# Kernel tuning notes

Measured on AMD Instinct MI355X. Metric: run time of the kernel, lower is better.

## Reference

```python
import jax, jax.numpy as jnp
import numpy as np

B, S, HID = 2, 4096, 1024
H, D = 16, 64

def rotate_half(x):
    x1, x2 = jnp.split(x, 2, axis=-1)
    return jnp.concatenate([-x2, x1], axis=-1)

def setup_inputs() -> dict:
    key = jax.random.key(0)
    ks = jax.random.split(key, 8)
    hidden_states = jax.random.normal(ks[0], (B, S, HID), dtype=jnp.float32)
    pos = jnp.arange(S, dtype=jnp.float32)[:, None]
    inv_freq = 1.0 / (10000.0 ** (jnp.arange(0, D, 2, dtype=jnp.float32) / D))
    freqs = pos * inv_freq[None, :]
    emb = jnp.concatenate([freqs, freqs], axis=-1)  # [S, D]
    cos = jnp.cos(emb)
    sin = jnp.sin(emb)
    W_rkv = jax.random.normal(ks[1], (3 * H * D, HID), dtype=jnp.float32) * 0.02
    W_o = jax.random.normal(ks[2], (HID, H * D), dtype=jnp.float32) * 0.02
    # match torch init: uniform(-8,-5), uniform(-1,1), uniform(0.2,0.8)
    time_decay = jax.random.uniform(ks[3], (H, D), minval=-8.0, maxval=-5.0, dtype=jnp.float32)
    time_first = jax.random.uniform(ks[4], (H, D), minval=-1.0, maxval=1.0, dtype=jnp.float32)
    time_mix = jax.random.uniform(ks[5], (1, 1, HID), minval=0.2, maxval=0.8, dtype=jnp.float32)
    return {"hidden_states": hidden_states, "cos": cos, "sin": sin,
            "W_rkv": W_rkv, "W_o": W_o, "time_decay": time_decay,
            "time_first": time_first, "time_mix": time_mix}

def reference(hidden_states, cos, sin, W_rkv, W_o, time_decay, time_first, time_mix):
    b, s, hid = hidden_states.shape
    # token-shift time mixing
    xx = jnp.concatenate([jnp.zeros_like(hidden_states[:, :1]), hidden_states[:, :-1]], axis=1)
    mixed = hidden_states * time_mix + xx * (1.0 - time_mix)
    rkv = jnp.einsum('bsh,oh->bso', mixed, W_rkv).reshape(b, s, 3, H, D)
    r = jax.nn.sigmoid(rkv[:, :, 0])  # [B,S,H,D]
    k = rkv[:, :, 1]
    v = rkv[:, :, 2]
    # rotary on r, k
    c = cos[None, :, None, :]
    sn = sin[None, :, None, :]
    r = r * c + rotate_half(r) * sn
    k = k * c + rotate_half(k) * sn
    # fast rwkv linear attention (parallel approximation)
    w = -jnp.exp(time_decay)
    kv = k * v  # [B,S,H,D]
    pos = jnp.arange(s, dtype=hidden_states.dtype)
    pos_diff = pos[:, None] - pos[None, :]  # [S,S]
    mask = pos_diff > 0  # i > j masked (per original code)
    avg_decay = jnp.mean(w)
    pd = jnp.where(mask, 0.0, pos_diff)
    dw = jnp.where(mask, 0.0, jnp.exp(avg_decay * -jnp.abs(pd)))
    dw = dw / (dw.sum(axis=1, keepdims=True) + 1e-8)
    weighted_kv = jnp.einsum('ij,bjhd->bihd', dw, kv)
    out = r * (time_first[None, None] * kv + weighted_kv)  # [B,S,H,D]
    out = out.reshape(b, s, H * D)
    return jnp.einsum('bso,ho->bsh', out, W_o)
```

## Files before the change

kernel.cpp:

```cpp
#include <hip/hip_runtime.h>
#include <math.h>

#define S_LEN 4096
#define HIDN  1024
#define NH    16
#define HD    64
#define BATCH 2
#define M_TOTAL (BATCH * S_LEN)
#define N_RKV   (3 * HIDN)
#define CS 128
#define NC (S_LEN / CS)

typedef __attribute__((ext_vector_type(8))) _Float16 f16x8;
typedef __attribute__((ext_vector_type(4))) float f32x4;
typedef __attribute__((ext_vector_type(4))) unsigned short u16x4;

__device__ __forceinline__ unsigned short f2h(float x) {
    _Float16 h = (_Float16)x;
    return *(unsigned short*)&h;
}
__device__ __forceinline__ float h2f(unsigned short b) {
    _Float16 h = *(_Float16*)&b;
    return (float)h;
}

__device__ __forceinline__ void load_lds16(const void* g, void* l) {
    __builtin_amdgcn_global_load_lds((const __attribute__((address_space(1))) void*)g,
                                     (__attribute__((address_space(3))) void*)l, 16, 0, 0);
}

__global__ void k_avg_decay(const float* __restrict__ td, float* __restrict__ a_out) {
    int t = threadIdx.x;
    double acc = 0.0;
    for (int i = t; i < NH * HD; i += 64) acc += exp((double)td[i]);
    for (int off = 32; off > 0; off >>= 1) acc += __shfl_down(acc, off, 64);
    if (t == 0) a_out[0] = (float)(acc / (double)(NH * HD));
}

__global__ __launch_bounds__(256)
void k_split_mix(const float* __restrict__ hs, const float* __restrict__ tm,
                 unsigned short* __restrict__ Ah) {
    int g = blockIdx.x * 256 + threadIdx.x;
    int kc = (g & 255) * 4;
    int m = g >> 8;
    float4 cur = *(const float4*)&hs[(size_t)m * HIDN + kc];
    float4 t4  = *(const float4*)&tm[kc];
    float4 prev = make_float4(0.f, 0.f, 0.f, 0.f);
    if (m & (S_LEN - 1)) prev = *(const float4*)&hs[(size_t)(m - 1) * HIDN + kc];
    u16x4 h;
    h.x = f2h(cur.x * t4.x + prev.x * (1.f - t4.x));
    h.y = f2h(cur.y * t4.y + prev.y * (1.f - t4.y));
    h.z = f2h(cur.z * t4.z + prev.z * (1.f - t4.z));
    h.w = f2h(cur.w * t4.w + prev.w * (1.f - t4.w));
    *(u16x4*)&Ah[(size_t)m * HIDN + kc] = h;
}

__global__ __launch_bounds__(256)
void k_split_w(const float* __restrict__ W, unsigned short* __restrict__ Wh) {
    int g = blockIdx.x * 256 + threadIdx.x;
    size_t o = (size_t)g * 4;
    float4 v = *(const float4*)&W[o];
    u16x4 h;
    h.x = f2h(v.x); h.y = f2h(v.y); h.z = f2h(v.z); h.w = f2h(v.w);
    *(u16x4*)&Wh[o] = h;
}

__device__ __forceinline__ f32x4 mfma16(f16x8 a, f16x8 b, f32x4 c) {
    return __builtin_amdgcn_mfma_f32_16x16x32_f16(a, b, c, 0, 0, 0);
}

template<int LDC, int NBX, bool HALF_OUT>
__global__ __launch_bounds__(256, 2)
void k_gemm_bt(const unsigned short* __restrict__ A,
               const unsigned short* __restrict__ Bm,
               void* __restrict__ Cv)
{
    __shared__ unsigned short smem[16384];
    const int tid  = threadIdx.x;
    const int lane = tid & 63;
    const int wave = tid >> 6;
    const int wm = wave >> 1, wn = wave & 1;

    const int cpx = gridDim.x >> 3;
    const int wg  = (blockIdx.x & 7) * cpx + (blockIdx.x >> 3);
    const int bx  = wg % NBX;
    const int by  = wg / NBX;
    const int m0 = by * 128;
    const int n0 = bx * 128;

    const unsigned short* segsrc[4];
    int segdst[4];
    {
        int rowoff = lane >> 2;
        int q = (lane & 3) ^ (rowoff & 3);
#pragma unroll
        for (int i = 0; i < 4; ++i) {
            int s = wave * 4 + i;
            const unsigned short* base = (s < 8) ? A : Bm;
            int row = (s < 8) ? (m0 + s * 16) : (n0 + (s - 8) * 16);
            segsrc[i] = base + (size_t)(row + rowoff) * 1024 + q * 8;
            segdst[i] = s * 512;
        }
    }

    const int lm = lane & 15;
    const int rq = lane >> 4;
    const int qx = rq ^ (lane & 3);
    int aoff[4], boff[4];
#pragma unroll
    for (int t = 0; t < 4; ++t) {
        aoff[t] = (wm * 64 + t * 16 + lm) * 32 + qx * 8;
        boff[t] = 4096 + (wn * 64 + t * 16 + lm) * 32 + qx * 8;
    }

    f32x4 acc[4][4] = {};

#pragma unroll
    for (int i = 0; i < 4; ++i) load_lds16(segsrc[i], smem + segdst[i]);

    int p = 0;
    for (int kt = 0; kt < 1024; kt += 32) {
        __syncthreads();
        if (kt + 32 < 1024) {
#pragma unroll
            for (int i = 0; i < 4; ++i)
                load_lds16(segsrc[i] + kt + 32, smem + ((p ^ 1) * 8192 + segdst[i]));
        }
        const unsigned short* sb = smem + p * 8192;
        f16x8 fa[4], fb[4];
#pragma unroll
        for (int t = 0; t < 4; ++t) {
            fa[t] = *(const f16x8*)(sb + aoff[t]);
            fb[t] = *(const f16x8*)(sb + boff[t]);
        }
#pragma unroll
        for (int mt = 0; mt < 4; ++mt)
#pragma unroll
            for (int nt = 0; nt < 4; ++nt)
                acc[mt][nt] = mfma16(fa[mt], fb[nt], acc[mt][nt]);
        p ^= 1;
    }

#pragma unroll
    for (int mt = 0; mt < 4; ++mt)
#pragma unroll
        for (int nt = 0; nt < 4; ++nt) {
            int col = n0 + wn * 64 + nt * 16 + lm;
#pragma unroll
            for (int r = 0; r < 4; ++r) {
                int row = m0 + wm * 64 + mt * 16 + rq * 4 + r;
                if constexpr (HALF_OUT)
                    ((unsigned short*)Cv)[(size_t)row * LDC + col] = f2h(acc[mt][nt][r]);
                else
                    ((float*)Cv)[(size_t)row * LDC + col] = acc[mt][nt][r];
            }
        }
}

__global__ __launch_bounds__(256)
void k_cb(const unsigned short* __restrict__ rkv,
          const float* __restrict__ cosp, const float* __restrict__ sinp,
          const float* __restrict__ a_ptr, float* __restrict__ Cb)
{
    __shared__ float Ls[4][64][4];
    int bid = blockIdx.x;
    int c  = bid & (NC - 1);
    int bh = bid >> 5;
    int b = bh >> 4, h = bh & 15;
    int lane = threadIdx.x & 63;
    int wave = threadIdx.x >> 6;
    int lm = lane & 15;
    int rs = lane >> 4;
    int d0 = lm * 4;
    float a = a_ptr[0];
    float sgn = (lm < 8) ? -1.f : 1.f;
    float ps0 = 0.f, ps1 = 0.f, ps2 = 0.f, ps3 = 0.f;
#pragma unroll
    for (int it = 0; it < 8; ++it) {
        int t = wave * 32 + it * 4 + rs;
        int s = c * CS + t;
        const unsigned short* rk = rkv + ((size_t)b * S_LEN + s) * N_RKV + h * 64 + d0;
        u16x4 k4 = *(const u16x4*)(rk + 1024);
        u16x4 v4 = *(const u16x4*)(rk + 2048);
        float4 cs4 = *(const float4*)&cosp[s * HD + d0];
        float4 sn4 = *(const float4*)&sinp[s * HD + d0];
        float e = expf(a * (float)t);
        float k0 = h2f(k4.x), k1 = h2f(k4.y), k2 = h2f(k4.z), k3 = h2f(k4.w);
        float kp0 = __shfl_xor(k0, 8, 64);
        float kp1 = __shfl_xor(k1, 8, 64);
        float kp2 = __shfl_xor(k2, 8, 64);
        float kp3 = __shfl_xor(k3, 8, 64);
        ps0 += e * (k0 * cs4.x + sgn * kp0 * sn4.x) * h2f(v4.x);
        ps1 += e * (k1 * cs4.y + sgn * kp1 * sn4.y) * h2f(v4.y);
        ps2 += e * (k2 * cs4.z + sgn * kp2 * sn4.z) * h2f(v4.z);
        ps3 += e * (k3 * cs4.w + sgn * kp3 * sn4.w) * h2f(v4.w);
    }
    Ls[wave][lane][0] = ps0; Ls[wave][lane][1] = ps1;
    Ls[wave][lane][2] = ps2; Ls[wave][lane][3] = ps3;
    __syncthreads();
    if (threadIdx.x < 64) {
        int d = threadIdx.x;
        int lmm = d >> 2, j = d & 3;
        float sum = 0.f;
#pragma unroll
        for (int wv = 0; wv < 4; ++wv)
#pragma unroll
            for (int r = 0; r < 4; ++r)
                sum += Ls[wv][r * 16 + lmm][j];
        Cb[((size_t)bh * NC + c) * 64 + d] = sum;
    }
}

__global__ __launch_bounds__(64)
void k_chunk_suffix(const float* __restrict__ Cb, const float* __restrict__ a_ptr,
                    float* __restrict__ Sb) {
    int bh = blockIdx.x;
    int d = threadIdx.x;
    float a = a_ptr[0];
    float eaCS = expf(a * (float)CS);
    float run = 0.f;
    Sb[(size_t)(bh * NC + NC - 1) * 64 + d] = 0.f;
    for (int c = NC - 2; c >= 0; --c) {
        run = Cb[(size_t)(bh * NC + c + 1) * 64 + d] + eaCS * run;
        Sb[(size_t)(bh * NC + c) * 64 + d] = run;
    }
}

__global__ __launch_bounds__(256)
void k_ztab(const float* __restrict__ a_ptr, float* __restrict__ Zt) {
    int i = blockIdx.x * 256 + threadIdx.x;
    if (i < S_LEN) {
        float a = a_ptr[0];
        float em1a = expm1f(a);
        Zt[i] = expm1f(a * (float)(S_LEN - i)) / em1a + 1e-8f;
    }
}

__global__ __launch_bounds__(256)
void k_wkv2(const unsigned short* __restrict__ rkv,
            const float* __restrict__ cosp, const float* __restrict__ sinp,
            const float* __restrict__ Sb, const float* __restrict__ a_ptr,
            const float* __restrict__ tf, const float* __restrict__ Zt,
            unsigned short* __restrict__ outH) {
    __shared__ unsigned short L[3 * 128 * 64];
    __shared__ float Tl[4][64];
    int bid = blockIdx.x;
    int c  = bid & (NC - 1);
    int bh = bid >> 5;
    int b = bh >> 4, h = bh & 15;
    int lane = threadIdx.x & 63;
    int wave = threadIdx.x >> 6;
    int s0 = c * CS;

#pragma unroll
    for (int i = 0; i < 12; ++i) {
        int seg = wave * 12 + i;
        int stream = seg >> 4;
        int rg = seg & 15;
        int row = rg * 8 + (lane >> 3);
        const unsigned short* src = rkv
            + ((size_t)b * S_LEN + s0 + row) * N_RKV + stream * 1024 + h * 64
            + (lane & 7) * 8;
        load_lds16(src, L + stream * 8192 + rg * 512);
    }
    __syncthreads();

    float a = a_ptr[0];
    float ea = expf(a);
    const unsigned short* Lr = L;
    const unsigned short* Lk = L + 8192;
    const unsigned short* Lv = L + 16384;
    float sgn = (lane < 32) ? -1.f : 1.f;
    int lx = lane ^ 32;

    float kvreg[32], rreg[32];
    float w = 1.f, T = 0.f;
#pragma unroll
    for (int t = 0; t < 32; ++t) {
        int row = wave * 32 + t;
        float r_ = h2f(Lr[row * 64 + lane]);
        float k_ = h2f(Lk[row * 64 + lane]);
        float kp = h2f(Lk[row * 64 + lx]);
        float v_ = h2f(Lv[row * 64 + lane]);
        float cs = cosp[(s0 + row) * HD + lane];
        float sn = sinp[(s0 + row) * HD + lane];
        float sig = 1.f / (1.f + expf(-r_));
        float sigp = __shfl_xor(sig, 32, 64);
        rreg[t]  = sig * cs + sgn * sigp * sn;
        kvreg[t] = (k_ * cs + sgn * kp * sn) * v_;
        T += w * kvreg[t];
        w *= ea;
    }
    Tl[wave][lane] = T;
    __syncthreads();

    float e32 = expf(a * 32.f);
    float S_run = Sb[(size_t)bid * 64 + lane] * expf(a * 32.f * (float)(3 - wave));
    float f = 1.f;
    for (int wp = wave + 1; wp < 4; ++wp) {
        S_run += f * Tl[wp][lane];
        f *= e32;
    }
    float tfv = tf[h * HD + lane];
#pragma unroll
    for (int t = 31; t >= 0; --t) {
        float kv = kvreg[t];
        S_run = kv + ea * S_run;
        int ig = s0 + wave * 32 + t;
        float Z = Zt[ig];
        float o = rreg[t] * (tfv * kv + S_run / Z);
        size_t m = (size_t)b * S_LEN + ig;
        outH[m * HIDN + h * HD + lane] = f2h(o);
    }
}

extern "C" void kernel_launch(void* const* d_in, const int* in_sizes, int n_in,
                              void* d_out, int out_size, void* d_ws, size_t ws_size,
                              hipStream_t stream) {
    const float* hs    = (const float*)d_in[0];
    const float* cosp  = (const float*)d_in[1];
    const float* sinp  = (const float*)d_in[2];
    const float* W_rkv = (const float*)d_in[3];
    const float* W_o   = (const float*)d_in[4];
    const float* td    = (const float*)d_in[5];
    const float* tf    = (const float*)d_in[6];
    const float* tm    = (const float*)d_in[7];
    float* out = (float*)d_out;

    char* w = (char*)d_ws;
    unsigned short* rkvH = (unsigned short*)w;
    unsigned short* Ah   = (unsigned short*)(w + 50331648);
    unsigned short* outH = (unsigned short*)(w + 50331648);
    unsigned short* Wrh  = (unsigned short*)(w + 67108864);
    unsigned short* Woh  = (unsigned short*)(w + 73400320);
    float*          Cb   = (float*)(w + 75497472);
    float*          Sb   = (float*)(w + 75759616);
    float*          a_ptr= (float*)(w + 76021760);
    float*          Zt   = Cb;

    k_avg_decay<<<1, 64, 0, stream>>>(td, a_ptr);

    k_split_mix<<<(M_TOTAL * HIDN / 4) / 256, 256, 0, stream>>>(hs, tm, Ah);
    k_split_w<<<(N_RKV * HIDN / 4) / 256, 256, 0, stream>>>(W_rkv, Wrh);
    k_split_w<<<(HIDN * HIDN / 4) / 256, 256, 0, stream>>>(W_o, Woh);

    k_gemm_bt<N_RKV, 24, true><<<1536, 256, 0, stream>>>(Ah, Wrh, rkvH);

    k_cb<<<BATCH * NH * NC, 256, 0, stream>>>(rkvH, cosp, sinp, a_ptr, Cb);
    k_chunk_suffix<<<BATCH * NH, 64, 0, stream>>>(Cb, a_ptr, Sb);
    k_ztab<<<S_LEN / 256, 256, 0, stream>>>(a_ptr, Zt);
    k_wkv2<<<BATCH * NH * NC, 256, 0, stream>>>(rkvH, cosp, sinp, Sb, a_ptr, tf, Zt, outH);

    k_gemm_bt<HIDN, 8, false><<<512, 256, 0, stream>>>(outH, Woh, out);
}
```

Baseline: 239.8 us.

## Replace RKV projection GEMM with 256x192-tile, 8-wave phased pipelined kernel

Adds a new 512-thread GEMM for the RKV projection that uses 256x192 output tiles with a 64-wide K step and double-buffered LDS. It interleaves async global-to-LDS staging with four MFMA phases per stage, using explicit waitcnt, sched barriers and setprio. The aim is to raise data reuse per tile and hide load latency better than the generic 128x128 kernel, at the cost of more LDS, register pressure and hand-tuned scheduling fragility. It also precomputes the reciprocal of the normalizer table so the WKV kernel multiplies instead of dividing.

```diff
diff --git a/kernel.cpp b/kernel.cpp
--- a/kernel.cpp
+++ b/kernel.cpp
@@ -69,6 +69,122 @@
     return __builtin_amdgcn_mfma_f32_16x16x32_f16(a, b, c, 0, 0, 0);
 }
 
+#define SBAR  do { __builtin_amdgcn_sched_barrier(0); __builtin_amdgcn_s_barrier(); \
+                   __builtin_amdgcn_sched_barrier(0); } while (0)
+#define LGKM0 do { asm volatile("s_waitcnt lgkmcnt(0)" ::: "memory"); \
+                   __builtin_amdgcn_sched_barrier(0); } while (0)
+#define VMC(n) asm volatile("s_waitcnt vmcnt(" #n ")" ::: "memory")
+
+__global__ __launch_bounds__(512, 2)
+void k_gemm1_8ph(const unsigned short* __restrict__ A,
+                 const unsigned short* __restrict__ Bm,
+                 unsigned short* __restrict__ C)
+{
+    __shared__ unsigned short smem[57344];
+    const int tid  = threadIdx.x;
+    const int lane = tid & 63;
+    const int wv   = tid >> 6;
+    const int wm = wv >> 2, wn = wv & 3;
+    const int lm = lane & 15, rq = lane >> 4;
+    const int swz = (lm & 7) << 4;
+
+    const int cpx = gridDim.x >> 3;
+    const int wg  = (blockIdx.x & 7) * cpx + (blockIdx.x >> 3);
+    const int bx  = wg & 15;
+    const int by  = wg >> 4;
+    const int m0 = by * 256, n0 = bx * 192;
+
+    const int srow = 8 * wv + (lane >> 3);
+    const int scol = ((lane & 7) ^ (lane >> 3)) * 8;
+    const unsigned short* sA = A  + (size_t)(m0 + srow) * 1024 + scol;
+    const unsigned short* sB = Bm + (size_t)(n0 + srow) * 1024 + scol;
+    unsigned short* dA = smem + wv * 512;
+    unsigned short* dB = smem + 16384 + wv * 512;
+
+#define STG_A(u, T, bf) load_lds16(sA + (u)*65536 + (T)*64, dA + (bf)*28672 + (u)*4096)
+#define STG_B(u, T, bf) load_lds16(sB + (u)*65536 + (T)*64, dB + (bf)*28672 + (u)*4096)
+
+    const int arow = (wm * 128 + lm) * 128 + rq * 16;
+    int boff[3][2];
+#pragma unroll
+    for (int nt = 0; nt < 3; ++nt)
+#pragma unroll
+        for (int kk = 0; kk < 2; ++kk)
+            boff[nt][kk] = (((wn * 48 + nt * 16 + lm) * 128 + rq * 16 + kk * 64) ^ swz);
+
+    f16x8 aF[2][2], bF[3][2];
+    f32x4 acc[8][3] = {};
+
+#define READ_A(q, bf) { const char* Ab = (const char*)smem + (bf)*57344; \
+    _Pragma("unroll") for (int m2 = 0; m2 < 2; ++m2) \
+    _Pragma("unroll") for (int kk = 0; kk < 2; ++kk) \
+        aF[m2][kk] = *(const f16x8*)(Ab + ((arow + (q)*4096 + m2*2048 + kk*64) ^ swz)); }
+
+#define READ_B(bf) { const char* Bb = (const char*)smem + (bf)*57344 + 32768; \
+    _Pragma("unroll") for (int nt = 0; nt < 3; ++nt) \
+    _Pragma("unroll") for (int kk = 0; kk < 2; ++kk) \
+        bF[nt][kk] = *(const f16x8*)(Bb + boff[nt][kk]); }
+
+#define MMQ(q) { __builtin_amdgcn_s_setprio(1); \
+    _Pragma("unroll") for (int kk = 0; kk < 2; ++kk) \
+    _Pragma("unroll") for (int m2 = 0; m2 < 2; ++m2) \
+    _Pragma("unroll") for (int nt = 0; nt < 3; ++nt) \
+        acc[(q)*2+m2][nt] = mfma16(aF[m2][kk], bF[nt][kk], acc[(q)*2+m2][nt]); \
+    __builtin_amdgcn_s_setprio(0); }
+
+    STG_A(0,0,0); STG_A(1,0,0); STG_A(2,0,0); STG_A(3,0,0);
+    STG_B(0,0,0); STG_B(1,0,0); STG_B(2,0,0);
+    STG_B(0,1,1); STG_B(1,1,1); STG_B(2,1,1);
+    STG_A(0,1,1); STG_A(2,1,1);
+    VMC(5);
+    SBAR;
+
+    for (int it = 0; it < 8; ++it) {
+        const int t = 2 * it;
+        const bool st = (it < 7);
+        READ_A(0, 0); READ_B(0);
+        STG_A(1, t + 1, 1); STG_A(3, t + 1, 1);
+        SBAR; LGKM0; MMQ(0); SBAR;
+        READ_A(1, 0);
+        if (st) { STG_B(0, t + 2, 0); STG_B(1, t + 2, 0); }
+        SBAR; LGKM0; MMQ(1); SBAR;
+        READ_A(2, 0);
+        if (st) { STG_B(2, t + 2, 0); STG_A(0, t + 2, 0); }
+        SBAR; LGKM0; MMQ(2); SBAR;
+        READ_A(3, 0);
+        if (st) { STG_A(2, t + 2, 0); }
+        SBAR; LGKM0; MMQ(3);
+        if (st) { VMC(5); } else { VMC(0); }
+        SBAR;
+        READ_A(0, 1); READ_B(1);
+        if (st) { STG_A(1, t + 2, 0); STG_A(3, t + 2, 0); }
+        SBAR; LGKM0; MMQ(0); SBAR;
+        READ_A(1, 1);
+        if (st) { STG_B(0, t + 3, 1); STG_B(1, t + 3, 1); }
+        SBAR; LGKM0; MMQ(1); SBAR;
+        READ_A(2, 1);
+        if (st) { STG_B(2, t + 3, 1); STG_A(0, t + 3, 1); }
+        SBAR; LGKM0; MMQ(2); SBAR;
+        READ_A(3, 1);
+        if (st) { STG_A(2, t + 3, 1); }
+        SBAR; LGKM0; MMQ(3);
+        if (st) { VMC(5); }
+        SBAR;
+    }
+
+#pragma unroll
+    for (int mt = 0; mt < 8; ++mt)
+#pragma unroll
+        for (int nt = 0; nt < 3; ++nt) {
+            int col = n0 + wn * 48 + nt * 16 + lm;
+#pragma unroll
+            for (int r = 0; r < 4; ++r) {
+                int row = m0 + wm * 128 + mt * 16 + rq * 4 + r;
+                C[(size_t)row * N_RKV + col] = f2h(acc[mt][nt][r]);
+            }
+        }
+}
+
 template<int LDC, int NBX, bool HALF_OUT>
 __global__ __launch_bounds__(256, 2)
 void k_gemm_bt(const unsigned short* __restrict__ A,
@@ -106,11 +222,11 @@
     const int lm = lane & 15;
     const int rq = lane >> 4;
     const int qx = rq ^ (lane & 3);
-    int aoff[4], boff[4];
+    int aoff[4], boff2[4];
 #pragma unroll
     for (int t = 0; t < 4; ++t) {
-        aoff[t] = (wm * 64 + t * 16 + lm) * 32 + qx * 8;
-        boff[t] = 4096 + (wn * 64 + t * 16 + lm) * 32 + qx * 8;
+        aoff[t]  = (wm * 64 + t * 16 + lm) * 32 + qx * 8;
+        boff2[t] = 4096 + (wn * 64 + t * 16 + lm) * 32 + qx * 8;
     }
 
     f32x4 acc[4][4] = {};
@@ -127,17 +243,17 @@
                 load_lds16(segsrc[i] + kt + 32, smem + ((p ^ 1) * 8192 + segdst[i]));
         }
         const unsigned short* sb = smem + p * 8192;
-        f16x8 fa[4], fb[4];
+        f16x8 fah[4], fb[4];
 #pragma unroll
         for (int t = 0; t < 4; ++t) {
-            fa[t] = *(const f16x8*)(sb + aoff[t]);
-            fb[t] = *(const f16x8*)(sb + boff[t]);
+            fah[t] = *(const f16x8*)(sb + aoff[t]);
+            fb[t]  = *(const f16x8*)(sb + boff2[t]);
         }
 #pragma unroll
         for (int mt = 0; mt < 4; ++mt)
 #pragma unroll
             for (int nt = 0; nt < 4; ++nt)
-                acc[mt][nt] = mfma16(fa[mt], fb[nt], acc[mt][nt]);
+                acc[mt][nt] = mfma16(fah[mt], fb[nt], acc[mt][nt]);
         p ^= 1;
     }
 
@@ -203,10 +319,10 @@
         int lmm = d >> 2, j = d & 3;
         float sum = 0.f;
 #pragma unroll
-        for (int wv = 0; wv < 4; ++wv)
+        for (int wvv = 0; wvv < 4; ++wvv)
 #pragma unroll
             for (int r = 0; r < 4; ++r)
-                sum += Ls[wv][r * 16 + lmm][j];
+                sum += Ls[wvv][r * 16 + lmm][j];
         Cb[((size_t)bh * NC + c) * 64 + d] = sum;
     }
 }
@@ -232,7 +348,7 @@
     if (i < S_LEN) {
         float a = a_ptr[0];
         float em1a = expm1f(a);
-        Zt[i] = expm1f(a * (float)(S_LEN - i)) / em1a + 1e-8f;
+        Zt[i] = 1.f / (expm1f(a * (float)(S_LEN - i)) / em1a + 1e-8f);
     }
 }
 
@@ -307,8 +423,7 @@
         float kv = kvreg[t];
         S_run = kv + ea * S_run;
         int ig = s0 + wave * 32 + t;
-        float Z = Zt[ig];
-        float o = rreg[t] * (tfv * kv + S_run / Z);
+        float o = rreg[t] * (tfv * kv + S_run * Zt[ig]);
         size_t m = (size_t)b * S_LEN + ig;
         outH[m * HIDN + h * HD + lane] = f2h(o);
     }
@@ -344,7 +459,7 @@
     k_split_w<<<(N_RKV * HIDN / 4) / 256, 256, 0, stream>>>(W_rkv, Wrh);
     k_split_w<<<(HIDN * HIDN / 4) / 256, 256, 0, stream>>>(W_o, Woh);
 
-    k_gemm_bt<N_RKV, 24, true><<<1536, 256, 0, stream>>>(Ah, Wrh, rkvH);
+    k_gemm1_8ph<<<512, 512, 0, stream>>>(Ah, Wrh, rkvH);
 
     k_cb<<<BATCH * NH * NC, 256, 0, stream>>>(rkvH, cosp, sinp, a_ptr, Cb);
     k_chunk_suffix<<<BATCH * NH, 64, 0, stream>>>(Cb, a_ptr, Sb);
```

Result: faster. 232.6 us (-3.0%).

## Replace RKV projection GEMM with 256x384-tile, 8-wave explicitly scheduled kernel

Applied to the files above, without the earlier changes.

The first projection GEMM moves from a 128x128-tile kernel with 1536 blocks to a new kernel that uses 256x384 tiles, 512 threads and 256 blocks. The new kernel double-buffers staged loads and interleaves them with two half-tile MFMA phases, using explicit barriers, waitcnt and setprio for scheduling. The larger tile is meant to cut global and LDS traffic per FLOP and hide load latency, at the cost of one block per CU and more register pressure. Separately, the Z table now stores reciprocals, so the WKV kernel multiplies instead of divides.

```diff
diff --git a/kernel.cpp b/kernel.cpp
--- a/kernel.cpp
+++ b/kernel.cpp
@@ -69,6 +69,105 @@
     return __builtin_amdgcn_mfma_f32_16x16x32_f16(a, b, c, 0, 0, 0);
 }
 
+#define SBAR  do { __builtin_amdgcn_sched_barrier(0); __builtin_amdgcn_s_barrier(); \
+                   __builtin_amdgcn_sched_barrier(0); } while (0)
+#define LGKM0 do { asm volatile("s_waitcnt lgkmcnt(0)" ::: "memory"); \
+                   __builtin_amdgcn_sched_barrier(0); } while (0)
+#define VMC(n) asm volatile("s_waitcnt vmcnt(" #n ")" ::: "memory")
+
+__global__ __launch_bounds__(512, 1)
+void k_gemm1_big(const unsigned short* __restrict__ A,
+                 const unsigned short* __restrict__ Bm,
+                 unsigned short* __restrict__ C)
+{
+    __shared__ unsigned short smem[40960];
+    const int tid  = threadIdx.x;
+    const int lane = tid & 63;
+    const int wv   = tid >> 6;
+    const int wm = wv >> 2, wn = wv & 3;
+    const int lm = lane & 15, rq = lane >> 4;
+
+    const int cpx = gridDim.x >> 3;
+    const int wg  = ((int)blockIdx.x & 7) * cpx + ((int)blockIdx.x >> 3);
+    const int bx  = wg & 7;
+    const int by  = wg >> 3;
+    const int m0 = by * 256, n0 = bx * 384;
+
+    const unsigned short* s1; int d1;
+    const unsigned short* s2[4]; int d2[4];
+    {
+        int r = lane & 15, kc = lane >> 4;
+        int u = (wv < 4) ? (4 + wv) : (8 + wv);
+        s1 = A + (size_t)(m0 + u * 16 + r) * 1024 + kc * 8;
+        d1 = u * 512;
+#pragma unroll
+        for (int j = 0; j < 4; ++j) {
+            int idx = wv * 4 + j;
+            int u2 = (idx < 4) ? idx : ((idx < 8) ? idx + 4 : idx + 8);
+            if (u2 < 16) {
+                s2[j] = A + (size_t)(m0 + u2 * 16 + r) * 1024 + kc * 8;
+                d2[j] = u2 * 512;
+            } else {
+                int f = u2 - 16;
+                s2[j] = Bm + (size_t)(n0 + f * 16 + r) * 1024 + kc * 8;
+                d2[j] = 8192 + f * 512;
+            }
+        }
+    }
+#define STG1(T, bf)    load_lds16(s1 + (T) * 32,    smem + (bf) * 20480 + d1)
+#define STG2(j, T, bf) load_lds16(s2[j] + (T) * 32, smem + (bf) * 20480 + d2[j])
+
+    const int aoff0 = (wm * 8) * 1024 + lane * 16;
+    const int boff0 = 16384 + (wn * 6) * 1024 + lane * 16;
+
+    f16x8 aF[4], bF[6];
+    f32x4 acc[8][6] = {};
+
+#define RD_B(bf) { const char* p_ = (const char*)smem + (bf) * 40960 + boff0; \
+    _Pragma("unroll") for (int nf = 0; nf < 6; ++nf) \
+        bF[nf] = *(const f16x8*)(p_ + nf * 1024); }
+#define RD_A(bf, half) { const char* p_ = (const char*)smem + (bf) * 40960 + aoff0 + (half) * 4096; \
+    _Pragma("unroll") for (int mf = 0; mf < 4; ++mf) \
+        aF[mf] = *(const f16x8*)(p_ + mf * 1024); }
+#define MM(half) { __builtin_amdgcn_s_setprio(1); \
+    _Pragma("unroll") for (int mf = 0; mf < 4; ++mf) \
+    _Pragma("unroll") for (int nf = 0; nf < 6; ++nf) \
+        acc[(half) * 4 + mf][nf] = mfma16(aF[mf], bF[nf], acc[(half) * 4 + mf][nf]); \
+    __builtin_amdgcn_s_setprio(0); }
+
+    STG1(0, 0); STG2(0, 0, 0); STG2(1, 0, 0); STG2(2, 0, 0); STG2(3, 0, 0);
+    STG2(0, 1, 1); STG2(1, 1, 1); STG2(2, 1, 1); STG2(3, 1, 1);
+    VMC(4);
+    SBAR;
+
+    for (int t = 0; t < 32; ++t) {
+        const int bf = t & 1;
+        RD_B(bf); RD_A(bf, 0);
+        if (t < 31) { STG1(t + 1, bf ^ 1); }
+        SBAR; LGKM0; MM(0);
+        if (t < 31) { VMC(5); } else { VMC(0); }
+        SBAR;
+        RD_A(bf, 1);
+        if (t < 30) { STG2(0, t + 2, bf); STG2(1, t + 2, bf);
+                      STG2(2, t + 2, bf); STG2(3, t + 2, bf); }
+        SBAR; LGKM0; MM(1);
+        if (t < 30) { VMC(5); } else if (t == 30) { VMC(1); } else { VMC(0); }
+        SBAR;
+    }
+
+#pragma unroll
+    for (int mf = 0; mf < 8; ++mf)
+#pragma unroll
+        for (int nf = 0; nf < 6; ++nf) {
+            int col = n0 + wn * 96 + nf * 16 + lm;
+#pragma unroll
+            for (int r = 0; r < 4; ++r) {
+                int row = m0 + wm * 128 + mf * 16 + rq * 4 + r;
+                C[(size_t)row * N_RKV + col] = f2h(acc[mf][nf][r]);
+            }
+        }
+}
+
 template<int LDC, int NBX, bool HALF_OUT>
 __global__ __launch_bounds__(256, 2)
 void k_gemm_bt(const unsigned short* __restrict__ A,
@@ -106,11 +205,11 @@
     const int lm = lane & 15;
     const int rq = lane >> 4;
     const int qx = rq ^ (lane & 3);
-    int aoff[4], boff[4];
+    int aoff[4], boff2[4];
 #pragma unroll
     for (int t = 0; t < 4; ++t) {
-        aoff[t] = (wm * 64 + t * 16 + lm) * 32 + qx * 8;
-        boff[t] = 4096 + (wn * 64 + t * 16 + lm) * 32 + qx * 8;
+        aoff[t]  = (wm * 64 + t * 16 + lm) * 32 + qx * 8;
+        boff2[t] = 4096 + (wn * 64 + t * 16 + lm) * 32 + qx * 8;
     }
 
     f32x4 acc[4][4] = {};
@@ -127,17 +226,17 @@
                 load_lds16(segsrc[i] + kt + 32, smem + ((p ^ 1) * 8192 + segdst[i]));
         }
         const unsigned short* sb = smem + p * 8192;
-        f16x8 fa[4], fb[4];
+        f16x8 fah[4], fb[4];
 #pragma unroll
         for (int t = 0; t < 4; ++t) {
-            fa[t] = *(const f16x8*)(sb + aoff[t]);
-            fb[t] = *(const f16x8*)(sb + boff[t]);
+            fah[t] = *(const f16x8*)(sb + aoff[t]);
+            fb[t]  = *(const f16x8*)(sb + boff2[t]);
         }
 #pragma unroll
         for (int mt = 0; mt < 4; ++mt)
 #pragma unroll
             for (int nt = 0; nt < 4; ++nt)
-                acc[mt][nt] = mfma16(fa[mt], fb[nt], acc[mt][nt]);
+                acc[mt][nt] = mfma16(fah[mt], fb[nt], acc[mt][nt]);
         p ^= 1;
     }
 
@@ -203,10 +302,10 @@
         int lmm = d >> 2, j = d & 3;
         float sum = 0.f;
 #pragma unroll
-        for (int wv = 0; wv < 4; ++wv)
+        for (int wvv = 0; wvv < 4; ++wvv)
 #pragma unroll
             for (int r = 0; r < 4; ++r)
-                sum += Ls[wv][r * 16 + lmm][j];
+                sum += Ls[wvv][r * 16 + lmm][j];
         Cb[((size_t)bh * NC + c) * 64 + d] = sum;
     }
 }
@@ -232,7 +331,7 @@
     if (i < S_LEN) {
         float a = a_ptr[0];
         float em1a = expm1f(a);
-        Zt[i] = expm1f(a * (float)(S_LEN - i)) / em1a + 1e-8f;
+        Zt[i] = 1.f / (expm1f(a * (float)(S_LEN - i)) / em1a + 1e-8f);
     }
 }
 
@@ -307,8 +406,7 @@
         float kv = kvreg[t];
         S_run = kv + ea * S_run;
         int ig = s0 + wave * 32 + t;
-        float Z = Zt[ig];
-        float o = rreg[t] * (tfv * kv + S_run / Z);
+        float o = rreg[t] * (tfv * kv + S_run * Zt[ig]);
         size_t m = (size_t)b * S_LEN + ig;
         outH[m * HIDN + h * HD + lane] = f2h(o);
     }
@@ -344,7 +442,7 @@
     k_split_w<<<(N_RKV * HIDN / 4) / 256, 256, 0, stream>>>(W_rkv, Wrh);
     k_split_w<<<(HIDN * HIDN / 4) / 256, 256, 0, stream>>>(W_o, Woh);
 
-    k_gemm_bt<N_RKV, 24, true><<<1536, 256, 0, stream>>>(Ah, Wrh, rkvH);
+    k_gemm1_big<<<256, 512, 0, stream>>>(Ah, Wrh, rkvH);
 
     k_cb<<<BATCH * NH * NC, 256, 0, stream>>>(rkvH, cosp, sinp, a_ptr, Cb);
     k_chunk_suffix<<<BATCH * NH, 64, 0, stream>>>(Cb, a_ptr, Sb);
```

Result: faster. 233.4 us (-2.7%).

## Replace RKV projection GEMM with 256x384-tile 32x32 MFMA triple-buffered kernel

Applied to the files above, without the earlier changes.

Adds a new GEMM kernel for the fused RKV projection that uses 512-thread blocks, 256x384 output tiles, 32x32x16 MFMA instructions, and a three-stage LDS ring with explicit vmcnt/lgkmcnt waits and raised wave priority around the MFMA blocks. The goal is more data reuse per LDS load and better overlap of global-to-LDS copies with compute than the previous 128x128 16x16 MFMA kernel. It also stores the reciprocal of the normaliser table so the WKV kernel multiplies instead of dividing. The larger tiles give only 256 blocks, which may under-fill the GPU and raise register pressure. The LDS layout has no swizzle, so bank conflicts are possible.

```diff
diff --git a/kernel.cpp b/kernel.cpp
--- a/kernel.cpp
+++ b/kernel.cpp
@@ -13,6 +13,7 @@
 
 typedef __attribute__((ext_vector_type(8))) _Float16 f16x8;
 typedef __attribute__((ext_vector_type(4))) float f32x4;
+typedef __attribute__((ext_vector_type(16))) float f32x16;
 typedef __attribute__((ext_vector_type(4))) unsigned short u16x4;
 
 __device__ __forceinline__ unsigned short f2h(float x) {
@@ -68,6 +69,106 @@
 __device__ __forceinline__ f32x4 mfma16(f16x8 a, f16x8 b, f32x4 c) {
     return __builtin_amdgcn_mfma_f32_16x16x32_f16(a, b, c, 0, 0, 0);
 }
+__device__ __forceinline__ f32x16 mfma32(f16x8 a, f16x8 b, f32x16 c) {
+    return __builtin_amdgcn_mfma_f32_32x32x16_f16(a, b, c, 0, 0, 0);
+}
+
+#define SBAR  do { __builtin_amdgcn_sched_barrier(0); __builtin_amdgcn_s_barrier(); \
+                   __builtin_amdgcn_sched_barrier(0); } while (0)
+#define FENCE_LGKM do { __builtin_amdgcn_sched_barrier(0); \
+                   asm volatile("s_waitcnt lgkmcnt(0)" ::: "memory"); \
+                   __builtin_amdgcn_sched_barrier(0); } while (0)
+#define VMC(n) asm volatile("s_waitcnt vmcnt(" #n ")" ::: "memory")
+
+__global__ __launch_bounds__(512, 2)
+void k_gemm1_32(const unsigned short* __restrict__ A,
+                const unsigned short* __restrict__ Bm,
+                unsigned short* __restrict__ C)
+{
+    __shared__ unsigned short smem[61440];
+    const int tid  = threadIdx.x;
+    const int lane = tid & 63;
+    const int wv   = tid >> 6;
+    const int wm = wv >> 2, wn = wv & 3;
+    const int l31 = lane & 31, lh = lane >> 5;
+
+    const int cpx = gridDim.x >> 3;
+    const int wg  = ((int)blockIdx.x & 7) * cpx + ((int)blockIdx.x >> 3);
+    const int bx  = wg & 7;
+    const int by  = wg >> 3;
+    const int m0 = by * 256, n0 = bx * 384;
+
+    const unsigned short* sA = A + (size_t)(m0 + wv * 32 + l31) * 1024 + lh * 8;
+    const int v0 = 3 * wv, v1 = 3 * wv + 1, v2 = 3 * wv + 2;
+    const unsigned short* sB0 = Bm + (size_t)(n0 + (v0 >> 1) * 32 + l31) * 1024 + (v0 & 1) * 16 + lh * 8;
+    const unsigned short* sB1 = Bm + (size_t)(n0 + (v1 >> 1) * 32 + l31) * 1024 + (v1 & 1) * 16 + lh * 8;
+    const unsigned short* sB2 = Bm + (size_t)(n0 + (v2 >> 1) * 32 + l31) * 1024 + (v2 & 1) * 16 + lh * 8;
+    const int dA0 = (2 * wv) * 512;
+    const int dA1 = (2 * wv + 1) * 512;
+    const int dB0 = 8192 + v0 * 512;
+    const int dB1 = 8192 + v1 * 512;
+    const int dB2 = 8192 + v2 * 512;
+
+#define STG_A(T, b) do { \
+    load_lds16(sA + (T) * 32,      smem + (b) * 20480 + dA0); \
+    load_lds16(sA + (T) * 32 + 16, smem + (b) * 20480 + dA1); } while (0)
+#define STG_B(T, b) do { \
+    load_lds16(sB0 + (T) * 32, smem + (b) * 20480 + dB0); \
+    load_lds16(sB1 + (T) * 32, smem + (b) * 20480 + dB1); \
+    load_lds16(sB2 + (T) * 32, smem + (b) * 20480 + dB2); } while (0)
+
+    const int aRd = wm * 8192 + lane * 16;
+    const int bRd = 16384 + wn * 6144 + lane * 16;
+
+    f16x8 aF[4], bF[3];
+    f32x16 acc[4][3] = {};
+
+#define RD(b, ks) { const char* p_ = (const char*)smem + (b) * 40960; \
+    _Pragma("unroll") for (int mf = 0; mf < 4; ++mf) \
+        aF[mf] = *(const f16x8*)(p_ + aRd + mf * 2048 + (ks) * 1024); \
+    _Pragma("unroll") for (int nf = 0; nf < 3; ++nf) \
+        bF[nf] = *(const f16x8*)(p_ + bRd + nf * 2048 + (ks) * 1024); }
+
+#define MM() { __builtin_amdgcn_s_setprio(1); \
+    _Pragma("unroll") for (int mf = 0; mf < 4; ++mf) \
+    _Pragma("unroll") for (int nf = 0; nf < 3; ++nf) \
+        acc[mf][nf] = mfma32(aF[mf], bF[nf], acc[mf][nf]); \
+    __builtin_amdgcn_s_setprio(0); }
+
+    STG_A(0, 0); STG_B(0, 0);
+    STG_A(1, 1); STG_B(1, 1);
+    VMC(5);
+    SBAR;
+
+    int bf = 0;
+    for (int t = 0; t < 32; ++t) {
+        int bs = bf + 2; if (bs >= 3) bs -= 3;
+        const bool st = (t < 30);
+        RD(bf, 0);
+        if (st) { STG_A(t + 2, bs); }
+        FENCE_LGKM;
+        MM();
+        RD(bf, 1);
+        if (st) { STG_B(t + 2, bs); }
+        FENCE_LGKM;
+        MM();
+        if (st) { VMC(5); } else { VMC(0); }
+        SBAR;
+        bf += 1; if (bf == 3) bf = 0;
+    }
+
+#pragma unroll
+    for (int mf = 0; mf < 4; ++mf)
+#pragma unroll
+        for (int nf = 0; nf < 3; ++nf) {
+            int col = n0 + wn * 96 + nf * 32 + l31;
+#pragma unroll
+            for (int reg = 0; reg < 16; ++reg) {
+                int row = m0 + wm * 128 + mf * 32 + (reg & 3) + 8 * (reg >> 2) + 4 * lh;
+                C[(size_t)row * N_RKV + col] = f2h(acc[mf][nf][reg]);
+            }
+        }
+}
 
 template<int LDC, int NBX, bool HALF_OUT>
 __global__ __launch_bounds__(256, 2)
@@ -106,11 +207,11 @@
     const int lm = lane & 15;
     const int rq = lane >> 4;
     const int qx = rq ^ (lane & 3);
-    int aoff[4], boff[4];
+    int aoff[4], boff2[4];
 #pragma unroll
     for (int t = 0; t < 4; ++t) {
-        aoff[t] = (wm * 64 + t * 16 + lm) * 32 + qx * 8;
-        boff[t] = 4096 + (wn * 64 + t * 16 + lm) * 32 + qx * 8;
+        aoff[t]  = (wm * 64 + t * 16 + lm) * 32 + qx * 8;
+        boff2[t] = 4096 + (wn * 64 + t * 16 + lm) * 32 + qx * 8;
     }
 
     f32x4 acc[4][4] = {};
@@ -127,17 +228,17 @@
                 load_lds16(segsrc[i] + kt + 32, smem + ((p ^ 1) * 8192 + segdst[i]));
         }
         const unsigned short* sb = smem + p * 8192;
-        f16x8 fa[4], fb[4];
+        f16x8 fah[4], fb[4];
 #pragma unroll
         for (int t = 0; t < 4; ++t) {
-            fa[t] = *(const f16x8*)(sb + aoff[t]);
-            fb[t] = *(const f16x8*)(sb + boff[t]);
+            fah[t] = *(const f16x8*)(sb + aoff[t]);
+            fb[t]  = *(const f16x8*)(sb + boff2[t]);
         }
 #pragma unroll
         for (int mt = 0; mt < 4; ++mt)
 #pragma unroll
             for (int nt = 0; nt < 4; ++nt)
-                acc[mt][nt] = mfma16(fa[mt], fb[nt], acc[mt][nt]);
+                acc[mt][nt] = mfma16(fah[mt], fb[nt], acc[mt][nt]);
         p ^= 1;
     }
 
@@ -203,10 +304,10 @@
         int lmm = d >> 2, j = d & 3;
         float sum = 0.f;
 #pragma unroll
-        for (int wv = 0; wv < 4; ++wv)
+        for (int wvv = 0; wvv < 4; ++wvv)
 #pragma unroll
             for (int r = 0; r < 4; ++r)
-                sum += Ls[wv][r * 16 + lmm][j];
+                sum += Ls[wvv][r * 16 + lmm][j];
         Cb[((size_t)bh * NC + c) * 64 + d] = sum;
     }
 }
@@ -232,7 +333,7 @@
     if (i < S_LEN) {
         float a = a_ptr[0];
         float em1a = expm1f(a);
-        Zt[i] = expm1f(a * (float)(S_LEN - i)) / em1a + 1e-8f;
+        Zt[i] = 1.f / (expm1f(a * (float)(S_LEN - i)) / em1a + 1e-8f);
     }
 }
 
@@ -307,8 +408,7 @@
         float kv = kvreg[t];
         S_run = kv + ea * S_run;
         int ig = s0 + wave * 32 + t;
-        float Z = Zt[ig];
-        float o = rreg[t] * (tfv * kv + S_run / Z);
+        float o = rreg[t] * (tfv * kv + S_run * Zt[ig]);
         size_t m = (size_t)b * S_LEN + ig;
         outH[m * HIDN + h * HD + lane] = f2h(o);
     }
@@ -344,7 +444,7 @@
     k_split_w<<<(N_RKV * HIDN / 4) / 256, 256, 0, stream>>>(W_rkv, Wrh);
     k_split_w<<<(HIDN * HIDN / 4) / 256, 256, 0, stream>>>(W_o, Woh);
 
-    k_gemm_bt<N_RKV, 24, true><<<1536, 256, 0, stream>>>(Ah, Wrh, rkvH);
+    k_gemm1_32<<<256, 512, 0, stream>>>(Ah, Wrh, rkvH);
 
     k_cb<<<BATCH * NH * NC, 256, 0, stream>>>(rkvH, cosp, sinp, a_ptr, Cb);
     k_chunk_suffix<<<BATCH * NH, 64, 0, stream>>>(Cb, a_ptr, Sb);
```

Result: faster. 234.8 us (-2.1%).
